# Kernel optimization log

Hardware: AMD Instinct MI355X
Metric: run time of the kernel (lower is better)

The kernel has to match this reference:

```python
import jax, jax.numpy as jnp
import numpy as np

B, S, H, DH, RD = 4, 512, 8, 64, 64
DM = H * DH  # hidden_size = 512


def setup_inputs() -> dict:
    key = jax.random.key(0)
    ks = jax.random.split(key, 8)
    x = jax.random.normal(ks[0], (B, S, DM), dtype=jnp.float32)
    graph_matrix = jax.random.randint(ks[1], (B, S, S), 0, 2).astype(jnp.int32)
    rel_embeddings = jax.random.normal(ks[2], (B, S, S, RD), dtype=jnp.float32)
    scale = 0.02
    Wq = jax.random.normal(ks[3], (DM, DM), dtype=jnp.float32) * scale
    Wk = jax.random.normal(ks[4], (DM, DM), dtype=jnp.float32) * scale
    Wv = jax.random.normal(ks[5], (DM, DM), dtype=jnp.float32) * scale
    Wr = jax.random.normal(ks[6], (DH, RD), dtype=jnp.float32) * scale
    br = jnp.zeros((DH,), dtype=jnp.float32)
    return {"input_tensor": x, "graph_matrix": graph_matrix,
            "rel_embeddings": rel_embeddings, "Wq": Wq, "Wk": Wk,
            "Wv": Wv, "Wr": Wr, "br": br}


def reference(input_tensor, graph_matrix, rel_embeddings, Wq, Wk, Wv, Wr, br):
    b, s, dm = input_tensor.shape
    h, dh = H, dm // H

    def heads(t):  # (b,s,dm) -> (b,h,s,dh)
        return t.reshape(b, s, h, dh).transpose(0, 2, 1, 3)

    q = heads(input_tensor @ Wq.T)
    k = heads(input_tensor @ Wk.T)
    v = heads(input_tensor @ Wv.T)

    # rel_to_hidden: (b,s,s,rel_dim) -> (b,s,s,dh); shared across heads
    rel_h = rel_embeddings @ Wr.T + br

    # matmul_rel(q, k, rel) == q.k^T + sum_d q[...,q_pos,d] * rel[...,q_pos,k_pos,d]
    # computed WITHOUT materializing the (b,h,s,s,dh) intermediate
    scores = (jnp.einsum('bhqd,bhkd->bhqk', q, k)
              + jnp.einsum('bhqd,bqkd->bhqk', q, rel_h))
    scores = scores / (dh ** 0.5)

    # adjacency masking: (1 - graph) * -1e9, broadcast over heads
    neg_inf_mask = (1.0 - graph_matrix.astype(scores.dtype)) * -1e9
    scores = scores + neg_inf_mask[:, None, :, :]

    probs = jax.nn.softmax(scores, axis=-1)  # dropout = identity at inference
    ctx = jnp.einsum('bhqk,bhkd->bqhd', probs, v).reshape(b, s, dm)
    return ctx
```

## Files before the change

### kernel.cpp

```cpp
#include <hip/hip_runtime.h>


typedef __attribute__((ext_vector_type(4))) float f32x4;
typedef __attribute__((ext_vector_type(8))) short s16x8;
typedef __attribute__((ext_vector_type(4))) unsigned short u16x4;
typedef __attribute__((ext_vector_type(8))) unsigned short u16x8;

typedef const __attribute__((address_space(1))) unsigned int* gas_ptr;
typedef __attribute__((address_space(3))) unsigned int* las_ptr;

__device__ __forceinline__ void gload16(const void* g, void* l) {
  __builtin_amdgcn_global_load_lds((gas_ptr)g, (las_ptr)l, 16, 0, 0);
}

__device__ __forceinline__ unsigned short f2bf(float f) {
  union { float f; unsigned int u; } x; x.f = f;
  return (unsigned short)((x.u + 0x7fffu + ((x.u >> 16) & 1u)) >> 16);
}
__device__ __forceinline__ float bf2f(unsigned short u) {
  union { unsigned int u; float f; } x; x.u = ((unsigned int)u) << 16;
  return x.f;
}

__global__ __launch_bounds__(256) void prep_w(
    const float* __restrict__ Wq, const float* __restrict__ Wk,
    const float* __restrict__ Wv, const float* __restrict__ Wr,
    unsigned short* __restrict__ Wb) {
  int blk = blockIdx.x, t = threadIdx.x;
  if (blk < 768) {
    int i = (blk * 256 + t) * 4;
    const float* src = (i < 262144) ? Wq : (i < 524288 ? Wk : Wv);
    f32x4 v = *(const f32x4*)(src + (i & 262143));
    u16x4 u; u.x = f2bf(v.x); u.y = f2bf(v.y); u.z = f2bf(v.z); u.w = f2bf(v.w);
    *(u16x4*)(Wb + i) = u;
  } else {
    int o = (blk - 768) * 256 + t;
    int c = o & 511, n = o >> 9, h = n >> 6, r = n & 63;
    float acc = 0.f;
#pragma unroll 8
    for (int d = 0; d < 64; ++d) acc += Wr[d * 64 + r] * Wq[(h * 64 + d) * 512 + c];
    Wb[3 * 262144 + o] = f2bf(acc);
  }
}

__global__ __launch_bounds__(256) void gemm_qkv64(
    const float* __restrict__ x, const unsigned short* __restrict__ Wb,
    unsigned short* __restrict__ Qb, unsigned short* __restrict__ Kb,
    unsigned short* __restrict__ Vt, unsigned short* __restrict__ QRb) {
  int z = blockIdx.z;
  const unsigned short* Bm = Wb + (long)z * 262144;
  int m0 = blockIdx.x * 64, n0 = blockIdx.y * 64;
  __shared__ alignas(16) unsigned short As[64][72];
  __shared__ alignas(16) unsigned short Bs[64][72];
  int t = threadIdx.x, lane = t & 63, w = t >> 6;
  int wm = (w >> 1) * 32, wn = (w & 1) * 32;
  int fr = lane & 15, fk = (lane >> 4) * 8;
  int sr = t >> 2, sc = (t & 3) * 16;
  f32x4 acc[2][2] = {};
  for (int k0 = 0; k0 < 512; k0 += 64) {
    __syncthreads();
    {
      const float* ap = x + (long)(m0 + sr) * 512 + k0 + sc;
      f32x4 v0 = *(const f32x4*)ap, v1 = *(const f32x4*)(ap + 4);
      f32x4 v2 = *(const f32x4*)(ap + 8), v3 = *(const f32x4*)(ap + 12);
      u16x8 u0, u1;
      u0[0] = f2bf(v0.x); u0[1] = f2bf(v0.y); u0[2] = f2bf(v0.z); u0[3] = f2bf(v0.w);
      u0[4] = f2bf(v1.x); u0[5] = f2bf(v1.y); u0[6] = f2bf(v1.z); u0[7] = f2bf(v1.w);
      u1[0] = f2bf(v2.x); u1[1] = f2bf(v2.y); u1[2] = f2bf(v2.z); u1[3] = f2bf(v2.w);
      u1[4] = f2bf(v3.x); u1[5] = f2bf(v3.y); u1[6] = f2bf(v3.z); u1[7] = f2bf(v3.w);
      *(u16x8*)&As[sr][sc] = u0;
      *(u16x8*)&As[sr][sc + 8] = u1;
      const unsigned short* bp = Bm + (long)(n0 + sr) * 512 + k0 + sc;
      *(u16x8*)&Bs[sr][sc] = *(const u16x8*)bp;
      *(u16x8*)&Bs[sr][sc + 8] = *(const u16x8*)(bp + 8);
    }
    __syncthreads();
#pragma unroll
    for (int kh = 0; kh < 2; ++kh) {
      s16x8 a0 = *(const s16x8*)&As[wm + fr][32 * kh + fk];
      s16x8 a1 = *(const s16x8*)&As[wm + 16 + fr][32 * kh + fk];
      s16x8 b0 = *(const s16x8*)&Bs[wn + fr][32 * kh + fk];
      s16x8 b1 = *(const s16x8*)&Bs[wn + 16 + fr][32 * kh + fk];
      acc[0][0] = __builtin_amdgcn_mfma_f32_16x16x32_bf16(a0, b0, acc[0][0], 0, 0, 0);
      acc[0][1] = __builtin_amdgcn_mfma_f32_16x16x32_bf16(a0, b1, acc[0][1], 0, 0, 0);
      acc[1][0] = __builtin_amdgcn_mfma_f32_16x16x32_bf16(a1, b0, acc[1][0], 0, 0, 0);
      acc[1][1] = __builtin_amdgcn_mfma_f32_16x16x32_bf16(a1, b1, acc[1][1], 0, 0, 0);
    }
  }
  int rbase = (lane >> 4) * 4;
#pragma unroll
  for (int i = 0; i < 2; ++i)
#pragma unroll
    for (int j = 0; j < 2; ++j)
#pragma unroll
      for (int jj = 0; jj < 4; ++jj) {
        int row = m0 + wm + 16 * i + rbase + jj;
        int cc  = n0 + wn + 16 * j + fr;
        int b = row >> 9, s = row & 511, h = cc >> 6, d = cc & 63;
        unsigned short val = f2bf(acc[i][j][jj]);
        if (z == 0)      Qb[(((long)(b * 8 + h)) * 512 + s) * 64 + d] = val;
        else if (z == 1) Kb[(((long)(b * 8 + h)) * 512 + s) * 64 + d] = val;
        else if (z == 2) Vt[(((long)(b * 8 + h)) * 64 + d) * 512 + s] = val;
        else             QRb[(long)row * 512 + cc] = val;
      }
}

#define G128_STAGE(MAT, SRC, LD, M0, K0)                                      \
  _Pragma("unroll") for (int is = 0; is < 4; ++is) {                          \
    int cb = (is * 4 + w) * 64;                                               \
    int fc = cb + lane;                                                       \
    int row = fc >> 3, cl = fc & 7;                                           \
    gload16(SRC + (long)(M0 + row) * LD + K0 + ((cl ^ (row & 7)) * 8),        \
            (char*)MAT + (size_t)fc * 16);                                    \
  }

#define G128_FRAGS(AF, BF)                                                    \
  _Pragma("unroll") for (int kk = 0; kk < 2; ++kk) {                          \
    _Pragma("unroll") for (int i = 0; i < 4; ++i) {                           \
      int ra = wm + 16 * i + fr;                                              \
      AF[kk][i] = *(const s16x8*)((const char*)As +                           \
                  ((size_t)ra * 8 + ((kk * 4 + g) ^ (ra & 7))) * 16);         \
      int rb = wn + 16 * i + fr;                                              \
      BF[kk][i] = *(const s16x8*)((const char*)Bs +                           \
                  ((size_t)rb * 8 + ((kk * 4 + g) ^ (rb & 7))) * 16);         \
    }                                                                         \
  }

__global__ __launch_bounds__(256) void gemm128_c16(
    const unsigned short* __restrict__ Ag, const unsigned short* __restrict__ Bg,
    unsigned short* __restrict__ Cb) {
  int z = blockIdx.z;
  const unsigned short* A = Ag + (long)z * 32768;
  const unsigned short* Bm = Bg + (long)z * 32768;
  long coff = (long)z * 262144;
  int m0 = blockIdx.x * 128, n0 = blockIdx.y * 128;
  __shared__ alignas(16) unsigned short As[128 * 64];
  __shared__ alignas(16) unsigned short Bs[128 * 64];
  int t = threadIdx.x, lane = t & 63, w = t >> 6;
  int wm = (w >> 1) * 64, wn = (w & 1) * 64;
  int fr = lane & 15, g = lane >> 4;
  f32x4 acc[4][4] = {};
  G128_STAGE(As, A, 64, m0, 0)
  G128_STAGE(Bs, Bm, 64, n0, 0)
  __syncthreads();
  s16x8 af[2][4], bf_[2][4];
  G128_FRAGS(af, bf_)
#pragma unroll
  for (int kk = 0; kk < 2; ++kk)
#pragma unroll
    for (int i = 0; i < 4; ++i)
#pragma unroll
      for (int j = 0; j < 4; ++j)
        acc[i][j] = __builtin_amdgcn_mfma_f32_16x16x32_bf16(af[kk][i], bf_[kk][j],
                                                            acc[i][j], 0, 0, 0);
  int rbase = g * 4;
#pragma unroll
  for (int i = 0; i < 4; ++i)
#pragma unroll
    for (int j = 0; j < 4; ++j)
#pragma unroll
      for (int jj = 0; jj < 4; ++jj) {
        long row = m0 + wm + 16 * i + rbase + jj;
        int cc   = n0 + wn + 16 * j + fr;
        Cb[coff + row * 512 + cc] = f2bf(acc[i][j][jj]);
      }
}

__global__ __launch_bounds__(256) void gemm_nt(
    const unsigned short* __restrict__ A, int lda, long sA,
    const unsigned short* __restrict__ Bm, int ldb, long sB,
    float* __restrict__ Cv, int ldc, int subC, long sC1, long sC2, int K) {
  int z = blockIdx.z;
  A  += (long)z * sA;
  Bm += (long)z * sB;
  long coff = (long)(z / subC) * sC1 + (long)(z % subC) * sC2;
  int m0 = blockIdx.x * 64, n0 = blockIdx.y * 64;
  __shared__ alignas(16) unsigned short As[64][40];
  __shared__ alignas(16) unsigned short Bs[64][40];
  int t = threadIdx.x, lane = t & 63, w = t >> 6;
  int wm = (w >> 1) * 32, wn = (w & 1) * 32;
  int fr = lane & 15, fk = (lane >> 4) * 8;
  int sr = t >> 2, sc = (t & 3) * 8;
  f32x4 acc[2][2] = {};
  for (int k0 = 0; k0 < K; k0 += 32) {
    __syncthreads();
    *(u16x8*)&As[sr][sc] = *(const u16x8*)(A + (long)(m0 + sr) * lda + k0 + sc);
    *(u16x8*)&Bs[sr][sc] = *(const u16x8*)(Bm + (long)(n0 + sr) * ldb + k0 + sc);
    __syncthreads();
    s16x8 a0 = *(const s16x8*)&As[wm + fr][fk];
    s16x8 a1 = *(const s16x8*)&As[wm + 16 + fr][fk];
    s16x8 b0 = *(const s16x8*)&Bs[wn + fr][fk];
    s16x8 b1 = *(const s16x8*)&Bs[wn + 16 + fr][fk];
    acc[0][0] = __builtin_amdgcn_mfma_f32_16x16x32_bf16(a0, b0, acc[0][0], 0, 0, 0);
    acc[0][1] = __builtin_amdgcn_mfma_f32_16x16x32_bf16(a0, b1, acc[0][1], 0, 0, 0);
    acc[1][0] = __builtin_amdgcn_mfma_f32_16x16x32_bf16(a1, b0, acc[1][0], 0, 0, 0);
    acc[1][1] = __builtin_amdgcn_mfma_f32_16x16x32_bf16(a1, b1, acc[1][1], 0, 0, 0);
  }
  int rbase = (lane >> 4) * 4;
#pragma unroll
  for (int i = 0; i < 2; ++i)
#pragma unroll
    for (int j = 0; j < 2; ++j)
#pragma unroll
      for (int jj = 0; jj < 4; ++jj) {
        long row = m0 + wm + 16 * i + rbase + jj;
        int cc   = n0 + wn + 16 * j + fr;
        Cv[coff + row * ldc + cc] = acc[i][j][jj];
      }
}

__global__ __launch_bounds__(256) void rel_fused(
    const float* __restrict__ rel, const int* __restrict__ graph,
    const unsigned short* __restrict__ Sqkb, const unsigned short* __restrict__ QRb,
    unsigned short* __restrict__ P) {
  int b = blockIdx.x >> 9, q = blockIdx.x & 511;
  __shared__ float s_lds[8][512];
  __shared__ unsigned short qr16[16][64];
  __shared__ int idxL[512];
  __shared__ int cntL[8];
  int t = threadIdx.x, lane = t & 63, w = t >> 6;

#pragma unroll
  for (int i = 0; i < 4; ++i) {
    f32x4 zv = {};
    *(f32x4*)&s_lds[0][t * 4 + i * 1024] = zv;
  }
  if (t < 64) {
    u16x8 v = *(const u16x8*)(QRb + ((long)(b * 512 + q)) * 512 + t * 8);
    *(u16x8*)&qr16[t >> 3][(t & 7) * 8] = v;
  } else if (t < 128) {
    u16x8 zv = {};
    *(u16x8*)&qr16[8 + ((t - 64) >> 3)][((t - 64) & 7) * 8] = zv;
  }
  const int* grow = graph + ((long)(b * 512 + q)) * 512;
  int gA = grow[t], gB = grow[t + 256];
  unsigned long long mA = __ballot(gA != 0);
  unsigned long long mB = __ballot(gB != 0);
  unsigned long long below = (lane == 63) ? ~0ull : ((1ull << (lane + 1)) - 1);
  below >>= 1;
  int pA = __popcll(mA & below), pB = __popcll(mB & below);
  if (lane == 0) { cntL[w] = __popcll(mA); cntL[4 + w] = __popcll(mB); }
  __syncthreads();
  int base[8];
  int nact = 0;
#pragma unroll
  for (int g2 = 0; g2 < 8; ++g2) { base[g2] = nact; nact += cntL[g2]; }
  if (gA) idxL[base[w] + pA] = t;
  if (gB) idxL[base[4 + w] + pB] = t + 256;
  __syncthreads();

  int fr = lane & 15, fk = (lane >> 4) * 8;
  s16x8 aq0 = *(const s16x8*)&qr16[fr][fk];
  s16x8 aq1 = *(const s16x8*)&qr16[fr][32 + fk];
  const float* rg = rel + ((long)(b * 512 + q)) * 32768;
  int nchunk = (nact + 63) >> 6;

  for (int c = 0; c < nchunk; ++c) {
    int slot = c * 64 + 16 * w + fr;
    int krow = (slot < nact) ? idxL[slot] : 0;
    const float* rp = rg + krow * 64;
    f32x4 r0 = *(const f32x4*)(rp + fk);
    f32x4 r1 = *(const f32x4*)(rp + fk + 4);
    f32x4 r2 = *(const f32x4*)(rp + 32 + fk);
    f32x4 r3 = *(const f32x4*)(rp + 32 + fk + 4);
    s16x8 b0, b1;
    b0[0] = (short)f2bf(r0.x); b0[1] = (short)f2bf(r0.y);
    b0[2] = (short)f2bf(r0.z); b0[3] = (short)f2bf(r0.w);
    b0[4] = (short)f2bf(r1.x); b0[5] = (short)f2bf(r1.y);
    b0[6] = (short)f2bf(r1.z); b0[7] = (short)f2bf(r1.w);
    b1[0] = (short)f2bf(r2.x); b1[1] = (short)f2bf(r2.y);
    b1[2] = (short)f2bf(r2.z); b1[3] = (short)f2bf(r2.w);
    b1[4] = (short)f2bf(r3.x); b1[5] = (short)f2bf(r3.y);
    b1[6] = (short)f2bf(r3.z); b1[7] = (short)f2bf(r3.w);
    f32x4 acc = {};
    acc = __builtin_amdgcn_mfma_f32_16x16x32_bf16(aq0, b0, acc, 0, 0, 0);
    acc = __builtin_amdgcn_mfma_f32_16x16x32_bf16(aq1, b1, acc, 0, 0, 0);
    if (lane < 32 && slot < nact) {
      int hb = (lane >> 4) * 4;
#pragma unroll
      for (int j = 0; j < 4; ++j) s_lds[hb + j][krow] = acc[j];
    }
  }
  __syncthreads();

  for (int h = w; h < 8; h += 4) {
    const unsigned short* srow = Sqkb + (((long)(b * 8 + h)) * 512 + q) * 512;
    float vals[8];
    float m = -3.0e38f;
#pragma unroll
    for (int i = 0; i < 8; ++i) {
      int k = lane + 64 * i;
      float msk = (1.0f - (float)grow[k]) * -1e9f;
      vals[i] = (s_lds[h][k] + bf2f(srow[k])) * 0.125f + msk;
      m = fmaxf(m, vals[i]);
    }
#pragma unroll
    for (int off = 32; off >= 1; off >>= 1) m = fmaxf(m, __shfl_xor(m, off));
    float sum = 0.f;
#pragma unroll
    for (int i = 0; i < 8; ++i) { vals[i] = __expf(vals[i] - m); sum += vals[i]; }
#pragma unroll
    for (int off = 32; off >= 1; off >>= 1) sum += __shfl_xor(sum, off);
    float inv = 1.0f / sum;
    unsigned short* Pg = P + (((long)(b * 8 + h)) * 512 + q) * 512;
#pragma unroll
    for (int i = 0; i < 8; ++i) Pg[lane + 64 * i] = f2bf(vals[i] * inv);
  }
}

extern "C" void kernel_launch(void* const* d_in, const int* in_sizes, int n_in,
                              void* d_out, int out_size, void* d_ws, size_t ws_size,
                              hipStream_t stream) {
  const float* x     = (const float*)d_in[0];
  const int*   graph = (const int*)d_in[1];
  const float* rel   = (const float*)d_in[2];
  const float* Wq    = (const float*)d_in[3];
  const float* Wk    = (const float*)d_in[4];
  const float* Wv    = (const float*)d_in[5];
  const float* Wr    = (const float*)d_in[6];
  float* out = (float*)d_out;

  char* wp = (char*)d_ws;
  unsigned short* Wb  = (unsigned short*)wp; wp += (size_t)2 * 4 * 262144;
  unsigned short* Qb  = (unsigned short*)wp; wp += (size_t)2 * 1048576;
  unsigned short* Kb  = (unsigned short*)wp; wp += (size_t)2 * 1048576;
  unsigned short* Vt  = (unsigned short*)wp; wp += (size_t)2 * 1048576;
  unsigned short* QRb = (unsigned short*)wp; wp += (size_t)2 * 1048576;
  unsigned short* Sqkb = (unsigned short*)wp; wp += (size_t)2 * 8388608;
  unsigned short* P   = (unsigned short*)wp; wp += (size_t)2 * 8388608;

  prep_w<<<1792, 256, 0, stream>>>(Wq, Wk, Wv, Wr, Wb);

  gemm_qkv64<<<dim3(32, 8, 4), 256, 0, stream>>>(x, Wb, Qb, Kb, Vt, QRb);

  gemm128_c16<<<dim3(4, 4, 32), 256, 0, stream>>>(Qb, Kb, Sqkb);

  rel_fused<<<2048, 256, 0, stream>>>(rel, graph, Sqkb, QRb, P);

  gemm_nt<<<dim3(8, 1, 32), 256, 0, stream>>>(
      P, 512, 262144L, Vt, 512, 32768L, out, 512, 8, 262144L, 64L, 512);
}
```

Before: 79.89 us.

## Pre-convert x to bf16 and use direct-to-LDS swizzled loads in QKV GEMM

The prep kernel now also converts the input activations to bf16 in a workspace buffer. The QKV projection GEMM then stages both operands with global_load_lds into XOR-swizzled LDS tiles instead of loading fp32 and converting per tile. Separately, the softmax stage seeds the score buffer with a large negative value for non-edges, so the explicit graph mask read and add are removed. The cost is an extra bf16 buffer write and read for x, plus a masking scheme that depends on unset scores staying at the sentinel value.

```diff
diff --git a/kernel.cpp b/kernel.cpp
--- a/kernel.cpp
+++ b/kernel.cpp
@@ -22,19 +22,25 @@
   return x.f;
 }
 
-__global__ __launch_bounds__(256) void prep_w(
-    const float* __restrict__ Wq, const float* __restrict__ Wk,
-    const float* __restrict__ Wv, const float* __restrict__ Wr,
+__global__ __launch_bounds__(256) void prep(
+    const float* __restrict__ x, const float* __restrict__ Wq,
+    const float* __restrict__ Wk, const float* __restrict__ Wv,
+    const float* __restrict__ Wr, unsigned short* __restrict__ xb,
     unsigned short* __restrict__ Wb) {
   int blk = blockIdx.x, t = threadIdx.x;
-  if (blk < 768) {
+  if (blk < 1024) {
     int i = (blk * 256 + t) * 4;
+    f32x4 v = *(const f32x4*)(x + i);
+    u16x4 u; u.x = f2bf(v.x); u.y = f2bf(v.y); u.z = f2bf(v.z); u.w = f2bf(v.w);
+    *(u16x4*)(xb + i) = u;
+  } else if (blk < 1792) {
+    int i = ((blk - 1024) * 256 + t) * 4;
     const float* src = (i < 262144) ? Wq : (i < 524288 ? Wk : Wv);
     f32x4 v = *(const f32x4*)(src + (i & 262143));
     u16x4 u; u.x = f2bf(v.x); u.y = f2bf(v.y); u.z = f2bf(v.z); u.w = f2bf(v.w);
     *(u16x4*)(Wb + i) = u;
   } else {
-    int o = (blk - 768) * 256 + t;
+    int o = (blk - 1792) * 256 + t;
     int c = o & 511, n = o >> 9, h = n >> 6, r = n & 63;
     float acc = 0.f;
 #pragma unroll 8
@@ -43,51 +49,71 @@
   }
 }
 
-__global__ __launch_bounds__(256) void gemm_qkv64(
-    const float* __restrict__ x, const unsigned short* __restrict__ Wb,
+#define G64_STAGE(MAT, SRC, LD, M0, K0)                                       \
+  _Pragma("unroll") for (int is = 0; is < 2; ++is) {                          \
+    int fc = is * 256 + w * 64 + lane;                                        \
+    int row = fc >> 3, cl = fc & 7;                                           \
+    gload16(SRC + (long)(M0 + row) * LD + K0 + ((cl ^ (row & 7)) * 8),        \
+            (char*)MAT + (size_t)fc * 16);                                    \
+  }
+#define G128_STAGE(MAT, SRC, LD, M0, K0)                                      \
+  _Pragma("unroll") for (int is = 0; is < 4; ++is) {                          \
+    int fc = (is * 4 + w) * 64 + lane;                                        \
+    int row = fc >> 3, cl = fc & 7;                                           \
+    gload16(SRC + (long)(M0 + row) * LD + K0 + ((cl ^ (row & 7)) * 8),        \
+            (char*)MAT + (size_t)fc * 16);                                    \
+  }
+
+#define G128_FRAGS(AF, BF)                                                    \
+  _Pragma("unroll") for (int kk = 0; kk < 2; ++kk) {                          \
+    _Pragma("unroll") for (int i = 0; i < 4; ++i) {                           \
+      int ra = wm + 16 * i + fr;                                              \
+      AF[kk][i] = *(const s16x8*)((const char*)As +                           \
+                  ((size_t)ra * 8 + ((kk * 4 + g) ^ (ra & 7))) * 16);         \
+      int rb = wn + 16 * i + fr;                                              \
+      BF[kk][i] = *(const s16x8*)((const char*)Bs +                           \
+                  ((size_t)rb * 8 + ((kk * 4 + g) ^ (rb & 7))) * 16);         \
+    }                                                                         \
+  }
+
+__global__ __launch_bounds__(256) void gemm_qkv_g(
+    const unsigned short* __restrict__ xb, const unsigned short* __restrict__ Wb,
     unsigned short* __restrict__ Qb, unsigned short* __restrict__ Kb,
     unsigned short* __restrict__ Vt, unsigned short* __restrict__ QRb) {
   int z = blockIdx.z;
   const unsigned short* Bm = Wb + (long)z * 262144;
   int m0 = blockIdx.x * 64, n0 = blockIdx.y * 64;
-  __shared__ alignas(16) unsigned short As[64][72];
-  __shared__ alignas(16) unsigned short Bs[64][72];
+  __shared__ alignas(16) unsigned short As[64 * 64];
+  __shared__ alignas(16) unsigned short Bs[64 * 64];
   int t = threadIdx.x, lane = t & 63, w = t >> 6;
   int wm = (w >> 1) * 32, wn = (w & 1) * 32;
-  int fr = lane & 15, fk = (lane >> 4) * 8;
-  int sr = t >> 2, sc = (t & 3) * 16;
+  int fr = lane & 15, g = lane >> 4;
   f32x4 acc[2][2] = {};
   for (int k0 = 0; k0 < 512; k0 += 64) {
     __syncthreads();
-    {
-      const float* ap = x + (long)(m0 + sr) * 512 + k0 + sc;
-      f32x4 v0 = *(const f32x4*)ap, v1 = *(const f32x4*)(ap + 4);
-      f32x4 v2 = *(const f32x4*)(ap + 8), v3 = *(const f32x4*)(ap + 12);
-      u16x8 u0, u1;
-      u0[0] = f2bf(v0.x); u0[1] = f2bf(v0.y); u0[2] = f2bf(v0.z); u0[3] = f2bf(v0.w);
-      u0[4] = f2bf(v1.x); u0[5] = f2bf(v1.y); u0[6] = f2bf(v1.z); u0[7] = f2bf(v1.w);
-      u1[0] = f2bf(v2.x); u1[1] = f2bf(v2.y); u1[2] = f2bf(v2.z); u1[3] = f2bf(v2.w);
-      u1[4] = f2bf(v3.x); u1[5] = f2bf(v3.y); u1[6] = f2bf(v3.z); u1[7] = f2bf(v3.w);
-      *(u16x8*)&As[sr][sc] = u0;
-      *(u16x8*)&As[sr][sc + 8] = u1;
-      const unsigned short* bp = Bm + (long)(n0 + sr) * 512 + k0 + sc;
-      *(u16x8*)&Bs[sr][sc] = *(const u16x8*)bp;
-      *(u16x8*)&Bs[sr][sc + 8] = *(const u16x8*)(bp + 8);
-    }
+    G64_STAGE(As, xb, 512, m0, k0)
+    G64_STAGE(Bs, Bm, 512, n0, k0)
     __syncthreads();
 #pragma unroll
     for (int kh = 0; kh < 2; ++kh) {
-      s16x8 a0 = *(const s16x8*)&As[wm + fr][32 * kh + fk];
-      s16x8 a1 = *(const s16x8*)&As[wm + 16 + fr][32 * kh + fk];
-      s16x8 b0 = *(const s16x8*)&Bs[wn + fr][32 * kh + fk];
-      s16x8 b1 = *(const s16x8*)&Bs[wn + 16 + fr][32 * kh + fk];
+      s16x8 a0, a1, b0, b1;
+      {
+        int ra = wm + fr;
+        a0 = *(const s16x8*)((const char*)As + ((size_t)ra * 8 + ((kh * 4 + g) ^ (ra & 7))) * 16);
+        int ra1 = wm + 16 + fr;
+        a1 = *(const s16x8*)((const char*)As + ((size_t)ra1 * 8 + ((kh * 4 + g) ^ (ra1 & 7))) * 16);
+        int rb = wn + fr;
+        b0 = *(const s16x8*)((const char*)Bs + ((size_t)rb * 8 + ((kh * 4 + g) ^ (rb & 7))) * 16);
+        int rb1 = wn + 16 + fr;
+        b1 = *(const s16x8*)((const char*)Bs + ((size_t)rb1 * 8 + ((kh * 4 + g) ^ (rb1 & 7))) * 16);
+      }
       acc[0][0] = __builtin_amdgcn_mfma_f32_16x16x32_bf16(a0, b0, acc[0][0], 0, 0, 0);
       acc[0][1] = __builtin_amdgcn_mfma_f32_16x16x32_bf16(a0, b1, acc[0][1], 0, 0, 0);
       acc[1][0] = __builtin_amdgcn_mfma_f32_16x16x32_bf16(a1, b0, acc[1][0], 0, 0, 0);
       acc[1][1] = __builtin_amdgcn_mfma_f32_16x16x32_bf16(a1, b1, acc[1][1], 0, 0, 0);
     }
   }
-  int rbase = (lane >> 4) * 4;
+  int rbase = g * 4;
 #pragma unroll
   for (int i = 0; i < 2; ++i)
 #pragma unroll
@@ -104,27 +130,6 @@
         else             QRb[(long)row * 512 + cc] = val;
       }
 }
-
-#define G128_STAGE(MAT, SRC, LD, M0, K0)                                      \
-  _Pragma("unroll") for (int is = 0; is < 4; ++is) {                          \
-    int cb = (is * 4 + w) * 64;                                               \
-    int fc = cb + lane;                                                       \
-    int row = fc >> 3, cl = fc & 7;                                           \
-    gload16(SRC + (long)(M0 + row) * LD + K0 + ((cl ^ (row & 7)) * 8),        \
-            (char*)MAT + (size_t)fc * 16);                                    \
-  }
-
-#define G128_FRAGS(AF, BF)                                                    \
-  _Pragma("unroll") for (int kk = 0; kk < 2; ++kk) {                          \
-    _Pragma("unroll") for (int i = 0; i < 4; ++i) {                           \
-      int ra = wm + 16 * i + fr;                                              \
-      AF[kk][i] = *(const s16x8*)((const char*)As +                           \
-                  ((size_t)ra * 8 + ((kk * 4 + g) ^ (ra & 7))) * 16);         \
-      int rb = wn + 16 * i + fr;                                              \
-      BF[kk][i] = *(const s16x8*)((const char*)Bs +                           \
-                  ((size_t)rb * 8 + ((kk * 4 + g) ^ (rb & 7))) * 16);         \
-    }                                                                         \
-  }
 
 __global__ __launch_bounds__(256) void gemm128_c16(
     const unsigned short* __restrict__ Ag, const unsigned short* __restrict__ Bg,
@@ -222,8 +227,8 @@
 
 #pragma unroll
   for (int i = 0; i < 4; ++i) {
-    f32x4 zv = {};
-    *(f32x4*)&s_lds[0][t * 4 + i * 1024] = zv;
+    f32x4 mv = {-8e9f, -8e9f, -8e9f, -8e9f};
+    *(f32x4*)&s_lds[0][t * 4 + i * 1024] = mv;
   }
   if (t < 64) {
     u16x8 v = *(const u16x8*)(QRb + ((long)(b * 512 + q)) * 512 + t * 8);
@@ -290,8 +295,7 @@
 #pragma unroll
     for (int i = 0; i < 8; ++i) {
       int k = lane + 64 * i;
-      float msk = (1.0f - (float)grow[k]) * -1e9f;
-      vals[i] = (s_lds[h][k] + bf2f(srow[k])) * 0.125f + msk;
+      vals[i] = (s_lds[h][k] + bf2f(srow[k])) * 0.125f;
       m = fmaxf(m, vals[i]);
     }
 #pragma unroll
@@ -321,6 +325,7 @@
   float* out = (float*)d_out;
 
   char* wp = (char*)d_ws;
+  unsigned short* xb  = (unsigned short*)wp; wp += (size_t)2 * 1048576;
   unsigned short* Wb  = (unsigned short*)wp; wp += (size_t)2 * 4 * 262144;
   unsigned short* Qb  = (unsigned short*)wp; wp += (size_t)2 * 1048576;
   unsigned short* Kb  = (unsigned short*)wp; wp += (size_t)2 * 1048576;
@@ -329,9 +334,9 @@
   unsigned short* Sqkb = (unsigned short*)wp; wp += (size_t)2 * 8388608;
   unsigned short* P   = (unsigned short*)wp; wp += (size_t)2 * 8388608;
 
-  prep_w<<<1792, 256, 0, stream>>>(Wq, Wk, Wv, Wr, Wb);
-
-  gemm_qkv64<<<dim3(32, 8, 4), 256, 0, stream>>>(x, Wb, Qb, Kb, Vt, QRb);
+  prep<<<2816, 256, 0, stream>>>(x, Wq, Wk, Wv, Wr, xb, Wb);
+
+  gemm_qkv_g<<<dim3(32, 8, 4), 256, 0, stream>>>(xb, Wb, Qb, Kb, Vt, QRb);
 
   gemm128_c16<<<dim3(4, 4, 32), 256, 0, stream>>>(Qb, Kb, Sqkb);
 
```

Measured after the change: 74.25 us. 7.1% less time.
